# Performance work log

Hardware: AMD Instinct MI355X
Metric: run time of the kernel (lower is better)

## Reference

```python
import jax, jax.numpy as jnp
import numpy as np
import math

B, S, D, H, DFF = 2, 2048, 1024, 16, 4096
DK = D // H
EPS = 1e-5


def setup_inputs() -> dict:
    key = jax.random.key(0)
    ks = jax.random.split(key, 8)
    s = 0.02
    return {
        "x": jax.random.normal(ks[0], (B, S, D), jnp.float32),
        "src_mask": jnp.ones((B, 1, 1, S), jnp.int32),
        "wq": jax.random.normal(ks[1], (D, D), jnp.float32) * s,
        "bq": jnp.zeros((D,), jnp.float32),
        "wk": jax.random.normal(ks[2], (D, D), jnp.float32) * s,
        "bk": jnp.zeros((D,), jnp.float32),
        "wv": jax.random.normal(ks[3], (D, D), jnp.float32) * s,
        "bv": jnp.zeros((D,), jnp.float32),
        "wo": jax.random.normal(ks[4], (D, D), jnp.float32) * s,
        "bo": jnp.zeros((D,), jnp.float32),
        "w1": jax.random.normal(ks[5], (DFF, D), jnp.float32) * s,
        "b1": jnp.zeros((DFF,), jnp.float32),
        "w2": jax.random.normal(ks[6], (D, DFF), jnp.float32) * s,
        "b2": jnp.zeros((D,), jnp.float32),
        "alpha1": jnp.ones((1,), jnp.float32),
        "bias1": jnp.ones((1,), jnp.float32),
        "alpha2": jnp.ones((1,), jnp.float32),
        "bias2": jnp.ones((1,), jnp.float32),
    }


def _layernorm(x, alpha, bias):
    # Faithful to source: unbiased std (ddof=1), divide by (std + eps),
    # scalar alpha/bias both initialized to 1.
    mean = jnp.mean(x, axis=-1, keepdims=True)
    std = jnp.std(x, axis=-1, keepdims=True, ddof=1)
    return alpha * (x - mean) / (std + EPS) + bias


def _mha(x, wq, bq, wk, bk, wv, bv, wo, bo):
    q = (x @ wq.T + bq).reshape(B, S, H, DK).swapaxes(1, 2)  # b h s d
    k = (x @ wk.T + bk).reshape(B, S, H, DK).swapaxes(1, 2)
    v = (x @ wv.T + bv).reshape(B, S, H, DK).swapaxes(1, 2)
    scores = jnp.einsum("bhqd,bhkd->bhqk", q, k) / math.sqrt(DK)
    # NOTE: source calls masked_fill (out-of-place) and discards the result,
    # so the mask has NO effect. Reproduced faithfully: no masking here.
    attn = jax.nn.softmax(scores, axis=-1)
    out = jnp.einsum("bhqk,bhkd->bhqd", attn, v)
    out = out.swapaxes(1, 2).reshape(B, S, D)
    return out @ wo.T + bo


def reference(x, src_mask, wq, bq, wk, bk, wv, bv, wo, bo,
              w1, b1, w2, b2, alpha1, bias1, alpha2, bias2):
    # residual[0]: x + attn(norm(x)) (dropout=0 -> identity)
    h1 = x + _mha(_layernorm(x, alpha1, bias1), wq, bq, wk, bk, wv, bv, wo, bo)
    # residual[1]: h1 + ffn(norm(h1))
    n2 = _layernorm(h1, alpha2, bias2)
    ffn = (n2 @ w1.T + b1) @ w2.T + b2
    return h1 + ffn
```

## Files before the change

kernel.cpp:

```cpp
#include <hip/hip_runtime.h>
#include <stdint.h>

#define Bx   2
#define Sx   2048
#define Dx   1024
#define Hx   16
#define DKx  64
#define DFFx 4096
#define Mx   4096

typedef __attribute__((ext_vector_type(8))) short short8;
typedef __attribute__((ext_vector_type(4))) float f32x4;
typedef __attribute__((ext_vector_type(4))) unsigned short ushort4v;

__device__ __forceinline__ unsigned short f2b(float f) {
    union { float f; uint32_t u; } v; v.f = f;
    uint32_t u = v.u;
    u += 0x7fffu + ((u >> 16) & 1u);
    return (unsigned short)(u >> 16);
}

__device__ __forceinline__ float fexp2(float x) {
#if __has_builtin(__builtin_amdgcn_exp2f)
    return __builtin_amdgcn_exp2f(x);
#else
    return exp2f(x);
#endif
}

__global__ __launch_bounds__(256) void conv_f2b(const float4* __restrict__ in,
                                                ushort4v* __restrict__ out, int n4) {
    int i = blockIdx.x * blockDim.x + threadIdx.x;
    if (i >= n4) return;
    float4 v = in[i];
    ushort4v o;
    o.x = f2b(v.x); o.y = f2b(v.y); o.z = f2b(v.z); o.w = f2b(v.w);
    out[i] = o;
}

__global__ __launch_bounds__(256) void bias_concat(const float* __restrict__ bq,
                                                   const float* __restrict__ bk,
                                                   const float* __restrict__ bv,
                                                   float* __restrict__ o) {
    int i = blockIdx.x * blockDim.x + threadIdx.x;
    if (i >= 3072) return;
    o[i] = (i < 1024) ? bq[i] : (i < 2048 ? bk[i - 1024] : bv[i - 2048]);
}

__global__ __launch_bounds__(256) void layernorm_k(const float* __restrict__ x,
                                                   const float* __restrict__ alpha,
                                                   const float* __restrict__ beta,
                                                   unsigned short* __restrict__ out) {
    __shared__ float red[8];
    const int row = blockIdx.x;
    const int t = threadIdx.x, lane = t & 63, w = t >> 6;
    float4 v = ((const float4*)(x + (size_t)row * Dx))[t];
    float s = v.x + v.y + v.z + v.w;
    float q = v.x*v.x + v.y*v.y + v.z*v.z + v.w*v.w;
#pragma unroll
    for (int off = 1; off < 64; off <<= 1) {
        s += __shfl_xor(s, off);
        q += __shfl_xor(q, off);
    }
    if (lane == 0) { red[w] = s; red[4 + w] = q; }
    __syncthreads();
    s = red[0] + red[1] + red[2] + red[3];
    q = red[4] + red[5] + red[6] + red[7];
    const float mean = s * (1.0f / Dx);
    float var = (q - (float)Dx * mean * mean) * (1.0f / (Dx - 1));
    var = fmaxf(var, 0.0f);
    const float inv = alpha[0] / (sqrtf(var) + 1e-5f);
    const float bb = beta[0];
    ushort4v o;
    o.x = f2b((v.x - mean) * inv + bb);
    o.y = f2b((v.y - mean) * inv + bb);
    o.z = f2b((v.z - mean) * inv + bb);
    o.w = f2b((v.w - mean) * inv + bb);
    *(ushort4v*)(out + (size_t)row * Dx + t * 4) = o;
}

#define GLDS(gp, lp) __builtin_amdgcn_global_load_lds( \
    (const __attribute__((address_space(1))) unsigned int*)(gp), \
    (__attribute__((address_space(3))) unsigned int*)(lp), 16, 0, 0)

#define STAGE(buf, kt) do {                                                     \
    const int k0_ = (kt) << 5;                                                  \
    _Pragma("unroll")                                                           \
    for (int i_ = 0; i_ < MB/2 + (MB==2); ++i_) {                               \
      const int ca_ = (MB==4) ? (w*2 + i_) : w;                                 \
      GLDS(A + (size_t)(bm + ca_*16 + srow)*K + k0_ + skc*8, &As[buf][ca_*512]);\
    }                                                                           \
    _Pragma("unroll")                                                           \
    for (int i_ = 0; i_ < 2; ++i_) {                                            \
      const int cb_ = w*2 + i_;                                                 \
      GLDS(W + (size_t)(bn + cb_*16 + srow)*K + k0_ + skc*8, &Bs[buf][cb_*512]);\
    }                                                                           \
  } while (0)

template<int MODE, int BM>
__global__ __launch_bounds__(256) void gemm2(const short* __restrict__ A,
                                             const short* __restrict__ W,
                                             const float* __restrict__ bias,
                                             const float* __restrict__ res,
                                             void* __restrict__ Cout,
                                             int M, int N, int K) {
    constexpr int MB = BM / 32;
    __shared__ alignas(16) short As[2][BM * 32];
    __shared__ alignas(16) short Bs[2][128 * 32];
    const int t = threadIdx.x, lane = t & 63, w = t >> 6;
    const int bm = blockIdx.y * BM, bn = blockIdx.x * 128;
    const int wm = (w >> 1) * (BM / 2), wn = (w & 1) * 64;
    const int srow = lane >> 2, skc = lane & 3;

    f32x4 acc[MB][4] = {};
    const int nkt = K >> 5;

    STAGE(0, 0);
    __syncthreads();
    int cur = 0;
    for (int kt = 0; kt < nkt; ++kt) {
        if (kt + 1 < nkt) STAGE(cur ^ 1, kt + 1);
        const short* as = &As[cur][0];
        const short* bs = &Bs[cur][0];
        short8 af[MB], bfr[4];
#pragma unroll
        for (int mb = 0; mb < MB; ++mb)
            af[mb] = *(const short8*)&as[(wm + mb * 16 + (lane & 15)) * 32 + (lane >> 4) * 8];
#pragma unroll
        for (int nb = 0; nb < 4; ++nb)
            bfr[nb] = *(const short8*)&bs[(wn + nb * 16 + (lane & 15)) * 32 + (lane >> 4) * 8];
#pragma unroll
        for (int mb = 0; mb < MB; ++mb)
#pragma unroll
            for (int nb = 0; nb < 4; ++nb)
                acc[mb][nb] = __builtin_amdgcn_mfma_f32_16x16x32_bf16(af[mb], bfr[nb], acc[mb][nb], 0, 0, 0);
        __syncthreads();
        cur ^= 1;
    }

    const int r0 = (lane >> 4) * 4, c0 = lane & 15;
#pragma unroll
    for (int mb = 0; mb < MB; ++mb)
#pragma unroll
        for (int nb = 0; nb < 4; ++nb) {
            const int col = bn + wn + nb * 16 + c0;
            const float bv = bias[col];
            const int row0 = bm + wm + mb * 16 + r0;
            if (MODE == 0) {
#pragma unroll
                for (int r = 0; r < 4; ++r)
                    ((unsigned short*)Cout)[(size_t)(row0 + r) * N + col] = f2b(acc[mb][nb][r] + bv);
            } else {
#pragma unroll
                for (int r = 0; r < 4; ++r) {
                    const size_t idx = (size_t)(row0 + r) * N + col;
                    ((float*)Cout)[idx] = acc[mb][nb][r] + bv + res[idx];
                }
            }
        }
}

#define STG256(buf, kt) do {                                                     \
    const int k0_ = (kt) << 5;                                                   \
    _Pragma("unroll")                                                            \
    for (int i_ = 0; i_ < 2; ++i_) {                                             \
      const int c_ = i_ * 8 + w;                                                 \
      GLDS(A + (size_t)(bm + c_*16 + (lane>>2))*K + k0_ + (lane&3)*8,            \
           &As[buf][c_*512]);                                                    \
      GLDS(W + (size_t)(bn + c_*16 + (lane>>2))*K + k0_ + (lane&3)*8,            \
           &Bs[buf][c_*512]);                                                    \
    }                                                                            \
  } while (0)

template<int MODE>
__global__ __launch_bounds__(512, 2) void gemm256(const short* __restrict__ A,
                                                  const short* __restrict__ W,
                                                  const float* __restrict__ bias,
                                                  void* __restrict__ Cout,
                                                  int M, int N, int K,
                                                  unsigned short* __restrict__ Qout,
                                                  unsigned short* __restrict__ Kout,
                                                  unsigned short* __restrict__ Vout) {
    __shared__ alignas(16) short As[2][256 * 32];
    __shared__ alignas(16) short Bs[2][256 * 32];
    const int t = threadIdx.x, lane = t & 63, w = t >> 6;
    const int lo = lane & 15, hi = lane >> 4;
    const int bm = blockIdx.y * 256, bn = blockIdx.x * 256;
    const int wr = w >> 2, wc = w & 3;

    f32x4 acc[8][4] = {};
    const int nkt = K >> 5;

    STG256(0, 0);
    __syncthreads();
    int cur = 0;
    for (int kt = 0; kt < nkt; ++kt) {
        if (kt + 1 < nkt) STG256(cur ^ 1, kt + 1);
        const short* as = &As[cur][0];
        const short* bs = &Bs[cur][0];
        short8 bfr[4];
#pragma unroll
        for (int nb = 0; nb < 4; ++nb)
            bfr[nb] = *(const short8*)&bs[(wc * 64 + nb * 16 + lo) * 32 + hi * 8];
#pragma unroll
        for (int mh = 0; mh < 2; ++mh) {
            short8 af[4];
#pragma unroll
            for (int mb = 0; mb < 4; ++mb)
                af[mb] = *(const short8*)&as[(wr * 128 + mh * 64 + mb * 16 + lo) * 32 + hi * 8];
#pragma unroll
            for (int mb = 0; mb < 4; ++mb)
#pragma unroll
                for (int nb = 0; nb < 4; ++nb)
                    acc[mh * 4 + mb][nb] =
                        __builtin_amdgcn_mfma_f32_16x16x32_bf16(af[mb], bfr[nb], acc[mh * 4 + mb][nb], 0, 0, 0);
        }
        __syncthreads();
        cur ^= 1;
    }

#pragma unroll
    for (int mb = 0; mb < 8; ++mb)
#pragma unroll
        for (int nb = 0; nb < 4; ++nb) {
            const int col = bn + wc * 64 + nb * 16 + lo;
            const float bv = bias[col];
            const int row0 = bm + wr * 128 + mb * 16 + hi * 4;
            if (MODE == 0) {
#pragma unroll
                for (int r = 0; r < 4; ++r)
                    ((unsigned short*)Cout)[(size_t)(row0 + r) * N + col] = f2b(acc[mb][nb][r] + bv);
            } else {
                if (col < 1024) {
#pragma unroll
                    for (int r = 0; r < 4; ++r)
                        Qout[(size_t)(row0 + r) * 1024 + col] = f2b(acc[mb][nb][r] + bv);
                } else if (col < 2048) {
#pragma unroll
                    for (int r = 0; r < 4; ++r)
                        Kout[(size_t)(row0 + r) * 1024 + (col - 1024)] = f2b(acc[mb][nb][r] + bv);
                } else {
                    const int dk = col - 2048, hh = dk >> 6, dlo = dk & 63;
                    const int bb = row0 >> 11, s0 = row0 & 2047;
                    const int vrow = (bb * 16 + hh) * 64 + dlo;
                    ushort4v pv;
                    pv.x = f2b(acc[mb][nb][0] + bv);
                    pv.y = f2b(acc[mb][nb][1] + bv);
                    pv.z = f2b(acc[mb][nb][2] + bv);
                    pv.w = f2b(acc[mb][nb][3] + bv);
                    *(ushort4v*)&Vout[(size_t)vrow * Sx + s0] = pv;
                }
            }
        }
}

__global__ __launch_bounds__(256) void attn_fwd3(const short* __restrict__ Q,
                                                 const short* __restrict__ Kg,
                                                 const short* __restrict__ Vtg,
                                                 unsigned short* __restrict__ O) {
    __shared__ alignas(16) short Ks[64 * 64];
    __shared__ alignas(16) short Vs[64 * 64];
    __shared__ alignas(16) short Pl[4][16 * 64];
    const int t = threadIdx.x, lane = t & 63, w = t >> 6;
    const int bh = blockIdx.x;
    const int b = bh >> 4, h = bh & 15;
    const int q0 = blockIdx.y * 64 + w * 16;
    const int lo = lane & 15, hi = lane >> 4;

    short8 qf[2];
#pragma unroll
    for (int kf = 0; kf < 2; ++kf)
        qf[kf] = *(const short8*)&Q[(size_t)(b * Sx + q0 + lo) * Dx + h * DKx + kf * 32 + hi * 8];

    f32x4 o_[4] = {};
    f32x4 l_acc = {};
    short8 ones;
#pragma unroll
    for (int j = 0; j < 8; ++j) ones[j] = (short)0x3F80;

    const int srow = t >> 2;
    const int scol2 = (t & 3) * 32;
    const int swz = (srow & 7) << 4;
    const short* Kbase = Kg + (size_t)(b * Sx) * Dx + h * DKx;
    const short* Vbase = Vtg + (size_t)(bh * 64 + srow) * Sx;
    char* KsB = (char*)Ks;
    char* VsB = (char*)Vs;
    char* PwB = (char*)&Pl[w][0];

    short8 kr0, kr1, vr0, vr1;
    {
        const short* kp = Kbase + (size_t)srow * Dx + (t & 3) * 16;
        kr0 = *(const short8*)kp; kr1 = *(const short8*)(kp + 8);
        const short* vp = Vbase + (t & 3) * 16;
        vr0 = *(const short8*)vp; vr1 = *(const short8*)(vp + 8);
    }

    const float cexp = 0.18033688011112042f;

    for (int kt = 0; kt < Sx / 64; ++kt) {
        __syncthreads();
        *(short8*)(KsB + ((srow * 128 + scol2) ^ swz)) = kr0;
        *(short8*)(KsB + ((srow * 128 + scol2 + 16) ^ swz)) = kr1;
        *(short8*)(VsB + ((srow * 128 + scol2) ^ swz)) = vr0;
        *(short8*)(VsB + ((srow * 128 + scol2 + 16) ^ swz)) = vr1;
        __syncthreads();
        if (kt + 1 < Sx / 64) {
            const short* kp = Kbase + (size_t)((kt + 1) * 64 + srow) * Dx + (t & 3) * 16;
            kr0 = *(const short8*)kp; kr1 = *(const short8*)(kp + 8);
            const short* vp = Vbase + (kt + 1) * 64 + (t & 3) * 16;
            vr0 = *(const short8*)vp; vr1 = *(const short8*)(vp + 8);
        }

        f32x4 s[4] = {};
#pragma unroll
        for (int nb = 0; nb < 4; ++nb) {
            const int key = nb * 16 + lo;
            const int ksw = (key & 7) << 4;
#pragma unroll
            for (int kf = 0; kf < 2; ++kf) {
                const short8 kfr = *(const short8*)(KsB + ((key * 128 + kf * 64 + hi * 16) ^ ksw));
                s[nb] = __builtin_amdgcn_mfma_f32_16x16x32_bf16(qf[kf], kfr, s[nb], 0, 0, 0);
            }
        }

#pragma unroll
        for (int nb = 0; nb < 4; ++nb) {
            const int k = nb * 16 + lo;
#pragma unroll
            for (int r = 0; r < 4; ++r) {
                const float p = fexp2(s[nb][r] * cexp);
                union { float f; uint32_t u; } cv; cv.f = p;
                const int qq = hi * 4 + r;
                *(short*)(PwB + ((qq * 128 + k * 2) ^ ((qq & 7) << 4))) = (short)(cv.u >> 16);
            }
        }

        short8 pa[2];
#pragma unroll
        for (int kc = 0; kc < 2; ++kc)
            pa[kc] = *(const short8*)(PwB + ((lo * 128 + kc * 64 + hi * 16) ^ ((lo & 7) << 4)));

        l_acc = __builtin_amdgcn_mfma_f32_16x16x32_bf16(pa[0], ones, l_acc, 0, 0, 0);
        l_acc = __builtin_amdgcn_mfma_f32_16x16x32_bf16(pa[1], ones, l_acc, 0, 0, 0);

#pragma unroll
        for (int d = 0; d < 4; ++d) {
            const int vd = d * 16 + lo;
            const int vsw = (vd & 7) << 4;
#pragma unroll
            for (int kc = 0; kc < 2; ++kc) {
                const short8 vf = *(const short8*)(VsB + ((vd * 128 + kc * 64 + hi * 16) ^ vsw));
                o_[d] = __builtin_amdgcn_mfma_f32_16x16x32_bf16(pa[kc], vf, o_[d], 0, 0, 0);
            }
        }
    }

#pragma unroll
    for (int d = 0; d < 4; ++d)
#pragma unroll
        for (int r = 0; r < 4; ++r) {
            const int qrow = b * Sx + q0 + hi * 4 + r;
            O[(size_t)qrow * Dx + h * DKx + d * 16 + lo] = f2b(o_[d][r] / l_acc[r]);
        }
}

extern "C" void kernel_launch(void* const* d_in, const int* in_sizes, int n_in,
                              void* d_out, int out_size, void* d_ws, size_t ws_size,
                              hipStream_t stream) {
    const float* x  = (const float*)d_in[0];
    const float* wq = (const float*)d_in[2];
    const float* bq = (const float*)d_in[3];
    const float* wk = (const float*)d_in[4];
    const float* bk = (const float*)d_in[5];
    const float* wv = (const float*)d_in[6];
    const float* bv = (const float*)d_in[7];
    const float* wo = (const float*)d_in[8];
    const float* bo = (const float*)d_in[9];
    const float* w1 = (const float*)d_in[10];
    const float* b1 = (const float*)d_in[11];
    const float* w2 = (const float*)d_in[12];
    const float* b2 = (const float*)d_in[13];
    const float* alpha1 = (const float*)d_in[14];
    const float* bias1  = (const float*)d_in[15];
    const float* alpha2 = (const float*)d_in[16];
    const float* bias2  = (const float*)d_in[17];
    float* out = (float*)d_out;

    short* ws   = (short*)d_ws;
    short* wqkv = ws;
    short* wob  = wqkv + 3145728;
    short* w1b  = wob  + 1048576;
    short* w2b  = w1b  + 4194304;
    short* n1   = w2b  + 4194304;
    short* Qb   = n1   + 4194304;
    short* Kb   = Qb   + 4194304;
    short* Vt   = Kb   + 4194304;
    short* f1   = Vt   + 4194304;
    float* h1   = (float*)(f1 + 16777216);
    float* bqkv = (float*)((char*)h1 + ((size_t)Mx * Dx * 4));
    short* ao = n1;
    short* n2 = n1;

    conv_f2b<<<1024, 256, 0, stream>>>((const float4*)wq, (ushort4v*)wqkv, 1 << 18);
    conv_f2b<<<1024, 256, 0, stream>>>((const float4*)wk, (ushort4v*)(wqkv + 1048576), 1 << 18);
    conv_f2b<<<1024, 256, 0, stream>>>((const float4*)wv, (ushort4v*)(wqkv + 2097152), 1 << 18);
    conv_f2b<<<1024, 256, 0, stream>>>((const float4*)wo, (ushort4v*)wob, 1 << 18);
    conv_f2b<<<4096, 256, 0, stream>>>((const float4*)w1, (ushort4v*)w1b, 1 << 20);
    conv_f2b<<<4096, 256, 0, stream>>>((const float4*)w2, (ushort4v*)w2b, 1 << 20);
    bias_concat<<<12, 256, 0, stream>>>(bq, bk, bv, bqkv);

    layernorm_k<<<Mx, 256, 0, stream>>>(x, alpha1, bias1, (unsigned short*)n1);

    gemm256<2><<<dim3(12, 16), 512, 0, stream>>>(n1, wqkv, bqkv, nullptr,
                                                 Mx, 3072, Dx,
                                                 (unsigned short*)Qb, (unsigned short*)Kb,
                                                 (unsigned short*)Vt);

    attn_fwd3<<<dim3(32, 32), 256, 0, stream>>>(Qb, Kb, Vt, (unsigned short*)ao);

    gemm2<1, 64><<<dim3(8, 64), 256, 0, stream>>>(ao, wob, bo, x, h1, Mx, Dx, Dx);

    layernorm_k<<<Mx, 256, 0, stream>>>(h1, alpha2, bias2, (unsigned short*)n2);

    gemm256<0><<<dim3(16, 16), 512, 0, stream>>>(n2, w1b, b1, f1,
                                                 Mx, DFFx, Dx, nullptr, nullptr, nullptr);
    gemm2<1, 64><<<dim3(8, 64), 256, 0, stream>>>(f1, w2b, b2, h1, out, Mx, Dx, DFFx);
}
```

Baseline: 403.9 us.

## Fuse weight conversions, add XCD-aware block remap, split-K the FFN down-projection

Merges the six weight conversions and the bias concat into a single launch to cut launch overhead. Remaps 1D block indices so that blocks landing on the same XCD share A rows, which should improve L2 reuse in all the GEMMs. The final K=4096 GEMM becomes a 128x128-tile split-K over two halves that write fp32 partials, followed by an elementwise epilogue that adds bias and residual. This trades a larger tile and fewer serial K iterations for extra partial-buffer traffic and one more kernel launch.

```diff
diff --git a/kernel.cpp b/kernel.cpp
--- a/kernel.cpp
+++ b/kernel.cpp
@@ -28,23 +28,38 @@
 #endif
 }
 
-__global__ __launch_bounds__(256) void conv_f2b(const float4* __restrict__ in,
-                                                ushort4v* __restrict__ out, int n4) {
-    int i = blockIdx.x * blockDim.x + threadIdx.x;
-    if (i >= n4) return;
-    float4 v = in[i];
-    ushort4v o;
-    o.x = f2b(v.x); o.y = f2b(v.y); o.z = f2b(v.z); o.w = f2b(v.w);
-    out[i] = o;
-}
-
-__global__ __launch_bounds__(256) void bias_concat(const float* __restrict__ bq,
-                                                   const float* __restrict__ bk,
-                                                   const float* __restrict__ bv,
-                                                   float* __restrict__ o) {
-    int i = blockIdx.x * blockDim.x + threadIdx.x;
-    if (i >= 3072) return;
-    o[i] = (i < 1024) ? bq[i] : (i < 2048 ? bk[i - 1024] : bv[i - 2048]);
+__global__ __launch_bounds__(256) void conv_all(
+    const float4* __restrict__ wq, const float4* __restrict__ wk,
+    const float4* __restrict__ wv, const float4* __restrict__ wo,
+    const float4* __restrict__ w1, const float4* __restrict__ w2,
+    const float4* __restrict__ bq, const float4* __restrict__ bk,
+    const float4* __restrict__ bv,
+    ushort4v* __restrict__ dqkv, ushort4v* __restrict__ dwo,
+    ushort4v* __restrict__ d1, ushort4v* __restrict__ d2,
+    float4* __restrict__ dbias) {
+    const int i = blockIdx.x * 256 + threadIdx.x;
+    const int S4 = 1 << 18;
+    if (i < 4 * S4) {
+        const float4* s; ushort4v* d;
+        if (i < S4)          { s = wq + i;            d = dqkv + i; }
+        else if (i < 2 * S4) { s = wk + (i - S4);     d = dqkv + i; }
+        else if (i < 3 * S4) { s = wv + (i - 2 * S4); d = dqkv + i; }
+        else                 { s = wo + (i - 3 * S4); d = dwo + (i - 3 * S4); }
+        const float4 v = *s;
+        ushort4v o; o.x = f2b(v.x); o.y = f2b(v.y); o.z = f2b(v.z); o.w = f2b(v.w);
+        *d = o;
+    } else if (i < 8 * S4) {
+        const float4 v = w1[i - 4 * S4];
+        ushort4v o; o.x = f2b(v.x); o.y = f2b(v.y); o.z = f2b(v.z); o.w = f2b(v.w);
+        d1[i - 4 * S4] = o;
+    } else if (i < 12 * S4) {
+        const float4 v = w2[i - 8 * S4];
+        ushort4v o; o.x = f2b(v.x); o.y = f2b(v.y); o.z = f2b(v.z); o.w = f2b(v.w);
+        d2[i - 8 * S4] = o;
+    } else if (i < 12 * S4 + 768) {
+        const int jn = i - 12 * S4;
+        dbias[jn] = (jn < 256) ? bq[jn] : (jn < 512 ? bk[jn - 256] : bv[jn - 512]);
+    }
 }
 
 __global__ __launch_bounds__(256) void layernorm_k(const float* __restrict__ x,
@@ -97,18 +112,20 @@
     }                                                                           \
   } while (0)
 
-template<int MODE, int BM>
+template<int BM>
 __global__ __launch_bounds__(256) void gemm2(const short* __restrict__ A,
                                              const short* __restrict__ W,
                                              const float* __restrict__ bias,
                                              const float* __restrict__ res,
-                                             void* __restrict__ Cout,
+                                             float* __restrict__ Cout,
                                              int M, int N, int K) {
     constexpr int MB = BM / 32;
     __shared__ alignas(16) short As[2][BM * 32];
     __shared__ alignas(16) short Bs[2][128 * 32];
     const int t = threadIdx.x, lane = t & 63, w = t >> 6;
-    const int bm = blockIdx.y * BM, bn = blockIdx.x * 128;
+    const int bb = blockIdx.x, xcd = bb & 7, jj = bb >> 3;
+    const int bn = (jj & 7) * 128;
+    const int bm = (xcd * 8 + (jj >> 3)) * BM;
     const int wm = (w >> 1) * (BM / 2), wn = (w & 1) * 64;
     const int srow = lane >> 2, skc = lane & 3;
 
@@ -146,18 +163,86 @@
             const int col = bn + wn + nb * 16 + c0;
             const float bv = bias[col];
             const int row0 = bm + wm + mb * 16 + r0;
-            if (MODE == 0) {
-#pragma unroll
-                for (int r = 0; r < 4; ++r)
-                    ((unsigned short*)Cout)[(size_t)(row0 + r) * N + col] = f2b(acc[mb][nb][r] + bv);
-            } else {
-#pragma unroll
-                for (int r = 0; r < 4; ++r) {
-                    const size_t idx = (size_t)(row0 + r) * N + col;
-                    ((float*)Cout)[idx] = acc[mb][nb][r] + bv + res[idx];
-                }
+#pragma unroll
+            for (int r = 0; r < 4; ++r) {
+                const size_t idx = (size_t)(row0 + r) * N + col;
+                Cout[idx] = acc[mb][nb][r] + bv + res[idx];
             }
         }
+}
+
+__global__ __launch_bounds__(256) void gemmsk(const short* __restrict__ A,
+                                              const short* __restrict__ W,
+                                              float* __restrict__ P0,
+                                              float* __restrict__ P1,
+                                              int K) {
+    constexpr int MB = 4;
+    __shared__ alignas(16) short As[2][128 * 32];
+    __shared__ alignas(16) short Bs[2][128 * 32];
+    const int t = threadIdx.x, lane = t & 63, w = t >> 6;
+    const int bb = blockIdx.x, xcd = bb & 7, jj = bb >> 3;
+    const int bn = (jj & 7) * 128;
+    const int p = (xcd << 3) | (jj >> 3);
+    const int bm = (p & 31) * 128;
+    const int kz = p >> 5;
+    float* __restrict__ P = kz ? P1 : P0;
+    const int wm = (w >> 1) * 64, wn = (w & 1) * 64;
+    const int srow = lane >> 2, skc = lane & 3;
+
+    f32x4 acc[MB][4] = {};
+    const int nkt = (K >> 1) >> 5;
+    const int kbeg = kz * nkt;
+
+    STAGE(0, kbeg);
+    __syncthreads();
+    int cur = 0;
+    for (int kt = kbeg; kt < kbeg + nkt; ++kt) {
+        if (kt + 1 < kbeg + nkt) STAGE(cur ^ 1, kt + 1);
+        const short* as = &As[cur][0];
+        const short* bs = &Bs[cur][0];
+        short8 af[MB], bfr[4];
+#pragma unroll
+        for (int mb = 0; mb < MB; ++mb)
+            af[mb] = *(const short8*)&as[(wm + mb * 16 + (lane & 15)) * 32 + (lane >> 4) * 8];
+#pragma unroll
+        for (int nb = 0; nb < 4; ++nb)
+            bfr[nb] = *(const short8*)&bs[(wn + nb * 16 + (lane & 15)) * 32 + (lane >> 4) * 8];
+#pragma unroll
+        for (int mb = 0; mb < MB; ++mb)
+#pragma unroll
+            for (int nb = 0; nb < 4; ++nb)
+                acc[mb][nb] = __builtin_amdgcn_mfma_f32_16x16x32_bf16(af[mb], bfr[nb], acc[mb][nb], 0, 0, 0);
+        __syncthreads();
+        cur ^= 1;
+    }
+
+    const int r0 = (lane >> 4) * 4, c0 = lane & 15;
+#pragma unroll
+    for (int mb = 0; mb < MB; ++mb)
+#pragma unroll
+        for (int nb = 0; nb < 4; ++nb) {
+            const int col = bn + wn + nb * 16 + c0;
+            const int row0 = bm + wm + mb * 16 + r0;
+#pragma unroll
+            for (int r = 0; r < 4; ++r)
+                P[(size_t)(row0 + r) * Dx + col] = acc[mb][nb][r];
+        }
+}
+
+__global__ __launch_bounds__(256) void epi2(const float4* __restrict__ p0,
+                                            const float4* __restrict__ p1,
+                                            const float4* __restrict__ b2,
+                                            const float4* __restrict__ h1,
+                                            float4* __restrict__ out) {
+    const int i = blockIdx.x * 256 + threadIdx.x;
+    const float4 bv = b2[i & 255];
+    const float4 a = p0[i], b = p1[i], h = h1[i];
+    float4 o;
+    o.x = a.x + b.x + h.x + bv.x;
+    o.y = a.y + b.y + h.y + bv.y;
+    o.z = a.z + b.z + h.z + bv.z;
+    o.w = a.w + b.w + h.w + bv.w;
+    out[i] = o;
 }
 
 #define STG256(buf, kt) do {                                                     \
@@ -178,6 +263,7 @@
                                                   const float* __restrict__ bias,
                                                   void* __restrict__ Cout,
                                                   int M, int N, int K,
+                                                  int nbn, int rpx,
                                                   unsigned short* __restrict__ Qout,
                                                   unsigned short* __restrict__ Kout,
                                                   unsigned short* __restrict__ Vout) {
@@ -185,7 +271,9 @@
     __shared__ alignas(16) short Bs[2][256 * 32];
     const int t = threadIdx.x, lane = t & 63, w = t >> 6;
     const int lo = lane & 15, hi = lane >> 4;
-    const int bm = blockIdx.y * 256, bn = blockIdx.x * 256;
+    const int bb = blockIdx.x, xcd = bb & 7, jj = bb >> 3;
+    const int bm = (xcd * rpx + jj / nbn) * 256;
+    const int bn = (jj % nbn) * 256;
     const int wr = w >> 2, wc = w & 3;
 
     f32x4 acc[8][4] = {};
@@ -241,8 +329,8 @@
                         Kout[(size_t)(row0 + r) * 1024 + (col - 1024)] = f2b(acc[mb][nb][r] + bv);
                 } else {
                     const int dk = col - 2048, hh = dk >> 6, dlo = dk & 63;
-                    const int bb = row0 >> 11, s0 = row0 & 2047;
-                    const int vrow = (bb * 16 + hh) * 64 + dlo;
+                    const int bbv = row0 >> 11, s0 = row0 & 2047;
+                    const int vrow = (bbv * 16 + hh) * 64 + dlo;
                     ushort4v pv;
                     pv.x = f2b(acc[mb][nb][0] + bv);
                     pv.y = f2b(acc[mb][nb][1] + bv);
@@ -400,29 +488,35 @@
     float* bqkv = (float*)((char*)h1 + ((size_t)Mx * Dx * 4));
     short* ao = n1;
     short* n2 = n1;
-
-    conv_f2b<<<1024, 256, 0, stream>>>((const float4*)wq, (ushort4v*)wqkv, 1 << 18);
-    conv_f2b<<<1024, 256, 0, stream>>>((const float4*)wk, (ushort4v*)(wqkv + 1048576), 1 << 18);
-    conv_f2b<<<1024, 256, 0, stream>>>((const float4*)wv, (ushort4v*)(wqkv + 2097152), 1 << 18);
-    conv_f2b<<<1024, 256, 0, stream>>>((const float4*)wo, (ushort4v*)wob, 1 << 18);
-    conv_f2b<<<4096, 256, 0, stream>>>((const float4*)w1, (ushort4v*)w1b, 1 << 20);
-    conv_f2b<<<4096, 256, 0, stream>>>((const float4*)w2, (ushort4v*)w2b, 1 << 20);
-    bias_concat<<<12, 256, 0, stream>>>(bq, bk, bv, bqkv);
+    float* p0 = (float*)n1;
+    float* p1 = (float*)Kb;
+
+    conv_all<<<12291, 256, 0, stream>>>((const float4*)wq, (const float4*)wk,
+                                        (const float4*)wv, (const float4*)wo,
+                                        (const float4*)w1, (const float4*)w2,
+                                        (const float4*)bq, (const float4*)bk,
+                                        (const float4*)bv,
+                                        (ushort4v*)wqkv, (ushort4v*)wob,
+                                        (ushort4v*)w1b, (ushort4v*)w2b,
+                                        (float4*)bqkv);
 
     layernorm_k<<<Mx, 256, 0, stream>>>(x, alpha1, bias1, (unsigned short*)n1);
 
-    gemm256<2><<<dim3(12, 16), 512, 0, stream>>>(n1, wqkv, bqkv, nullptr,
-                                                 Mx, 3072, Dx,
-                                                 (unsigned short*)Qb, (unsigned short*)Kb,
-                                                 (unsigned short*)Vt);
+    gemm256<2><<<192, 512, 0, stream>>>(n1, wqkv, bqkv, nullptr,
+                                        Mx, 3072, Dx, 12, 2,
+                                        (unsigned short*)Qb, (unsigned short*)Kb,
+                                        (unsigned short*)Vt);
 
     attn_fwd3<<<dim3(32, 32), 256, 0, stream>>>(Qb, Kb, Vt, (unsigned short*)ao);
 
-    gemm2<1, 64><<<dim3(8, 64), 256, 0, stream>>>(ao, wob, bo, x, h1, Mx, Dx, Dx);
+    gemm2<64><<<512, 256, 0, stream>>>(ao, wob, bo, x, h1, Mx, Dx, Dx);
 
     layernorm_k<<<Mx, 256, 0, stream>>>(h1, alpha2, bias2, (unsigned short*)n2);
 
-    gemm256<0><<<dim3(16, 16), 512, 0, stream>>>(n2, w1b, b1, f1,
-                                                 Mx, DFFx, Dx, nullptr, nullptr, nullptr);
-    gemm2<1, 64><<<dim3(8, 64), 256, 0, stream>>>(f1, w2b, b2, h1, out, Mx, Dx, DFFx);
-}
+    gemm256<0><<<256, 512, 0, stream>>>(n2, w1b, b1, f1,
+                                        Mx, DFFx, Dx, 16, 2, nullptr, nullptr, nullptr);
+
+    gemmsk<<<512, 256, 0, stream>>>(f1, w2b, p0, p1, DFFx);
+    epi2<<<4096, 256, 0, stream>>>((const float4*)p0, (const float4*)p1,
+                                   (const float4*)b2, (const float4*)h1, (float4*)out);
+}
```

Result: faster. 377.5 us (-6.5%).
